# Kernel tuning notes

Measured on AMD Instinct MI355X. Metric: run time of the kernel, lower is better.

The kernel has to match this reference:

```python
import jax, jax.numpy as jnp
import numpy as np

DIM = 128
KS = 7
HEADS = 4
HEAD_DIM = DIM // HEADS


def setup_inputs() -> dict:
    key = jax.random.key(0)
    ks = jax.random.split(key, 10)
    B, H, W, C = 4, 64, 64, DIM
    s = 0.02
    return {
        "x": jax.random.normal(ks[0], (B, H, W, C), jnp.float32),
        "qkv_w": jax.random.normal(ks[1], (C, 3 * C), jnp.float32) * s,
        "qkv_b": jnp.zeros((3 * C,), jnp.float32),
        "proj_w": jax.random.normal(ks[2], (C, C), jnp.float32) * s,
        "proj_b": jnp.zeros((C,), jnp.float32),
        "rpb": jax.random.normal(ks[3], (HEADS, 2 * KS - 1, 2 * KS - 1), jnp.float32) * s,
        "g1_w": jax.random.normal(ks[4], (C, C // 2), jnp.float32) * s,
        "g1_b": jnp.zeros((C // 2,), jnp.float32),
        "g2_w": jax.random.normal(ks[5], (C // 2, 1), jnp.float32) * s,
        "g2_b": jnp.zeros((1,), jnp.float32),
    }


def _neighborhood_attention(x, qkv_w, qkv_b, proj_w, proj_b, rpb):
    B, H, W, C = x.shape
    k = KS
    # qkv projection -> [B,H,W,3,heads,head_dim]
    qkv = (x @ qkv_w + qkv_b).reshape(B, H, W, 3, HEADS, HEAD_DIM)
    q = qkv[..., 0, :, :] * (HEAD_DIM ** -0.5)  # [B,H,W,h,d]
    kk = qkv[..., 1, :, :]
    v = qkv[..., 2, :, :]

    # Clamped sliding-window start indices (NATTEN semantics)
    sh = jnp.clip(jnp.arange(H) - k // 2, 0, H - k)  # [H]
    sw = jnp.clip(jnp.arange(W) - k // 2, 0, W - k)  # [W]
    idx_h = sh[:, None] + jnp.arange(k)[None, :]  # [H,k]
    idx_w = sw[:, None] + jnp.arange(k)[None, :]  # [W,k]

    # Gather neighborhood windows: [B,H,W,k,k,h,d]
    kwin = kk[:, idx_h[:, None, :, None], idx_w[None, :, None, :]]
    vwin = v[:, idx_h[:, None, :, None], idx_w[None, :, None, :]]

    # Relative position bias indices: (neighbor - query) + (k-1)
    bih = idx_h - jnp.arange(H)[:, None] + (k - 1)  # [H,k]
    biw = idx_w - jnp.arange(W)[:, None] + (k - 1)  # [W,k]
    # bias: [h,H,W,k,k] -> [H,W,h,k,k]
    bias = rpb[:, bih[:, None, :, None], biw[None, :, None, :]]
    bias = jnp.transpose(bias, (1, 2, 0, 3, 4))

    # scores: [B,H,W,h,k,k]
    scores = jnp.einsum('bxyhd,bxyklhd->bxyhkl', q, kwin) + bias[None]
    attn = jax.nn.softmax(scores.reshape(B, H, W, HEADS, k * k), axis=-1)
    attn = attn.reshape(B, H, W, HEADS, k, k)
    out = jnp.einsum('bxyhkl,bxyklhd->bxyhd', attn, vwin).reshape(B, H, W, C)
    return out @ proj_w + proj_b


def reference(x, qkv_w, qkv_b, proj_w, proj_b, rpb, g1_w, g1_b, g2_w, g2_b):
    attn_out = _neighborhood_attention(x, qkv_w, qkv_b, proj_w, proj_b, rpb)
    gate = jax.nn.sigmoid(jax.nn.relu(x @ g1_w + g1_b) @ g2_w + g2_b)  # [B,H,W,1]
    return attn_out * gate + x
```

## Files before the change

### kernel.cpp

```cpp
#include <hip/hip_runtime.h>
#include <hip/hip_bf16.h>
#include <math.h>

#define PIXELS 16384
#define C      128
#define KS     7
#define HEADS  4
#define HD     32
#define QSCALE 0.17677669529663687f

typedef __bf16 bf16x8 __attribute__((ext_vector_type(8)));
typedef __bf16 bf16x2 __attribute__((ext_vector_type(2)));
typedef float  f32x4  __attribute__((ext_vector_type(4)));
typedef float  f32x2  __attribute__((ext_vector_type(2)));

__device__ inline unsigned short f2bf(float f) {
    unsigned int u = __builtin_bit_cast(unsigned int, f);
    u += 0x7FFFu + ((u >> 16) & 1u);
    return (unsigned short)(u >> 16);
}
__device__ inline float bflo(unsigned int u) {
    return __builtin_bit_cast(float, u << 16);
}
__device__ inline float bfhi(unsigned int u) {
    return __builtin_bit_cast(float, u & 0xFFFF0000u);
}

__global__ __launch_bounds__(256) void prep_kernel(
    const float* __restrict__ qkv_w, const float* __restrict__ g1_w,
    const float* __restrict__ qkv_b, const float* __restrict__ g1_b,
    const float* __restrict__ proj_w,
    unsigned short* __restrict__ wT, unsigned short* __restrict__ pT,
    float* __restrict__ bias_ext)
{
    const int blk = blockIdx.x, tid = threadIdx.x;
    if (blk < 56) {
        int n = blk * 8 + (tid >> 5);
        int kq = tid & 31;
        float f0, f1, f2, f3;
        if (n < 384) {
            f0 = qkv_w[(kq*4+0)*384 + n]; f1 = qkv_w[(kq*4+1)*384 + n];
            f2 = qkv_w[(kq*4+2)*384 + n]; f3 = qkv_w[(kq*4+3)*384 + n];
        } else {
            int nn = n - 384;
            f0 = g1_w[(kq*4+0)*64 + nn]; f1 = g1_w[(kq*4+1)*64 + nn];
            f2 = g1_w[(kq*4+2)*64 + nn]; f3 = g1_w[(kq*4+3)*64 + nn];
        }
        ushort4 o; o.x = f2bf(f0); o.y = f2bf(f1); o.z = f2bf(f2); o.w = f2bf(f3);
        *(ushort4*)(wT + n*128 + kq*4) = o;
    } else if (blk < 72) {
        int n = (blk - 56) * 8 + (tid >> 5);
        int kq = tid & 31;
        ushort4 o;
        o.x = f2bf(proj_w[(kq*4+0)*128 + n]);
        o.y = f2bf(proj_w[(kq*4+1)*128 + n]);
        o.z = f2bf(proj_w[(kq*4+2)*128 + n]);
        o.w = f2bf(proj_w[(kq*4+3)*128 + n]);
        *(ushort4*)(pT + n*128 + kq*4) = o;
    } else {
        for (int idx = tid; idx < 448; idx += 256)
            bias_ext[idx] = (idx < 384) ? qkv_b[idx] : g1_b[idx - 384];
    }
}

__global__ __launch_bounds__(256) void gemm_qkvh_fused(
    const float* __restrict__ x, const unsigned short* __restrict__ wT,
    const float* __restrict__ bias_ext, const float* __restrict__ g2_w,
    const float* __restrict__ g2_b, unsigned short* __restrict__ qkvb,
    float* __restrict__ gate)
{
    __shared__ __align__(16) unsigned short As[64*128];
    __shared__ __align__(16) unsigned short Bs[64*128];
    __shared__ __align__(16) unsigned short Cs[64*64];
    const int grp = blockIdx.x;
    const int ntBeg = grp ? 4 : 0, ntEnd = grp ? 7 : 4;
    const int m0 = blockIdx.y * 64;
    const int tid = threadIdx.x;

#pragma unroll
    for (int it = 0; it < 4; it++) {
        int idx = tid + it*256, row = idx >> 4, c = idx & 15;
        const float* src = x + (size_t)(m0+row)*128 + c*8;
        float4 a = *(const float4*)src;
        float4 b2 = *(const float4*)(src + 4);
        uint4 v;
        v.x = (unsigned int)f2bf(a.x)  | ((unsigned int)f2bf(a.y)  << 16);
        v.y = (unsigned int)f2bf(a.z)  | ((unsigned int)f2bf(a.w)  << 16);
        v.z = (unsigned int)f2bf(b2.x) | ((unsigned int)f2bf(b2.y) << 16);
        v.w = (unsigned int)f2bf(b2.z) | ((unsigned int)f2bf(b2.w) << 16);
        *(uint4*)(As + row*128 + ((c ^ (row&7)) << 3)) = v;
    }

    const int wave = tid >> 6, lane = tid & 63;
    const int l15 = lane & 15, quad = lane >> 4;
    const int wm = (wave & 1) * 32, wn = (wave >> 1) * 32;

    for (int nt = ntBeg; nt < ntEnd; nt++) {
        const int n0 = nt * 64;
#pragma unroll
        for (int it = 0; it < 4; it++) {
            int idx = tid + it*256, row = idx >> 4, c = idx & 15;
            uint4 v = *(const uint4*)(wT + (size_t)(n0+row)*128 + c*8);
            *(uint4*)(Bs + row*128 + ((c ^ (row&7)) << 3)) = v;
        }
        __syncthreads();

        f32x4 acc[2][2] = {};
#pragma unroll
        for (int ks = 0; ks < 4; ks++) {
            bf16x8 af[2], bq[2];
#pragma unroll
            for (int mt = 0; mt < 2; mt++) {
                int m = wm + mt*16 + l15;
                af[mt] = *(const bf16x8*)(As + m*128 + (((ks*4+quad) ^ (m&7)) << 3));
            }
#pragma unroll
            for (int ntl = 0; ntl < 2; ntl++) {
                int n = wn + ntl*16 + l15;
                bq[ntl] = *(const bf16x8*)(Bs + n*128 + (((ks*4+quad) ^ (n&7)) << 3));
            }
#pragma unroll
            for (int mt = 0; mt < 2; mt++)
#pragma unroll
                for (int ntl = 0; ntl < 2; ntl++)
                    acc[mt][ntl] = __builtin_amdgcn_mfma_f32_16x16x32_bf16(
                        af[mt], bq[ntl], acc[mt][ntl], 0, 0, 0);
        }

        if (nt < 6) {
#pragma unroll
            for (int ntl = 0; ntl < 2; ntl++) {
                int nl = wn + ntl*16 + l15;
                int ng = n0 + nl;
                float qs = (ng < 128) ? QSCALE : 1.0f;
                float bv = bias_ext[ng];
#pragma unroll
                for (int mt = 0; mt < 2; mt++)
#pragma unroll
                    for (int r = 0; r < 4; r++) {
                        int ml = wm + mt*16 + quad*4 + r;
                        Cs[ml*64 + nl] = f2bf((acc[mt][ntl][r] + bv) * qs);
                    }
            }
            __syncthreads();
            int row = tid >> 2, part = tid & 3;
            uint4 a = *(const uint4*)(Cs + row*64 + part*16);
            uint4 b = *(const uint4*)(Cs + row*64 + part*16 + 8);
            unsigned short* dst = qkvb + (size_t)(m0+row)*384 + n0 + part*16;
            *(uint4*)dst = a;
            *(uint4*)(dst + 8) = b;
        } else {
            float* gpart = (float*)Cs;
            float rs[2][4];
#pragma unroll
            for (int mt = 0; mt < 2; mt++)
#pragma unroll
                for (int r = 0; r < 4; r++) rs[mt][r] = 0.0f;
#pragma unroll
            for (int ntl = 0; ntl < 2; ntl++) {
                int nl = wn + ntl*16 + l15;
                float bv = bias_ext[384 + nl];
                float gw = g2_w[nl];
#pragma unroll
                for (int mt = 0; mt < 2; mt++)
#pragma unroll
                    for (int r = 0; r < 4; r++) {
                        float h = acc[mt][ntl][r] + bv;
                        rs[mt][r] += fmaxf(h, 0.0f) * gw;
                    }
            }
#pragma unroll
            for (int off = 1; off <= 8; off <<= 1)
#pragma unroll
                for (int mt = 0; mt < 2; mt++)
#pragma unroll
                    for (int r = 0; r < 4; r++)
                        rs[mt][r] += __shfl_xor(rs[mt][r], off);
            if (l15 == 0) {
#pragma unroll
                for (int mt = 0; mt < 2; mt++)
#pragma unroll
                    for (int r = 0; r < 4; r++)
                        gpart[(wave >> 1)*64 + wm + mt*16 + quad*4 + r] = rs[mt][r];
            }
            __syncthreads();
            if (tid < 64) {
                float g = gpart[tid] + gpart[64 + tid] + g2_b[0];
                gate[m0 + tid] = 1.0f / (1.0f + __expf(-g));
            }
        }
    }
}

__global__ __launch_bounds__(128) void attn_kernel(
    const unsigned short* __restrict__ qkvb, const float* __restrict__ rpb,
    unsigned short* __restrict__ attnb)
{
    __shared__ __align__(16) unsigned short kvs[140 * 136];
    __shared__ float rpb_lds[2 * 169];

    const int blk = blockIdx.x;
    const int pr = blk & 1;
    const int tile = (blk >> 1) & 127;
    const int b = blk >> 8;
    const int ti0 = (tile >> 3) * 4, tj0 = (tile & 7) * 8;
    int wr0 = ti0 - 3; wr0 = wr0 < 0 ? 0 : (wr0 > 54 ? 54 : wr0);
    int wc0 = tj0 - 3; wc0 = wc0 < 0 ? 0 : (wc0 > 50 ? 50 : wc0);

    const int tid = threadIdx.x;
    const int hh = tid >> 6, lane = tid & 63;
    const int h = pr * 2 + hh;
    const int half = lane >> 5;
    const int p5 = lane & 31;
    const int pi = p5 >> 3, pj = p5 & 7;
    const int i = ti0 + pi, j = tj0 + pj;
    int sh = i - 3; sh = sh < 0 ? 0 : (sh > 57 ? 57 : sh);
    int sw = j - 3; sw = sw < 0 ? 0 : (sw > 57 ? 57 : sw);
    const int dr = sh - wr0, dc = sw - wc0;
    const size_t gp = (size_t)(((b << 6) + i) << 6) + j;

    unsigned int qu[8];
    const unsigned short* qptr = qkvb + gp * 384 + h * 32 + half * 16;
    *(uint4*)(qu + 0) = *(const uint4*)(qptr + 0);
    *(uint4*)(qu + 4) = *(const uint4*)(qptr + 8);

    float rpb_v[3];
#pragma unroll
    for (int t = 0; t < 3; t++) {
        int idx = tid + t * 128;
        rpb_v[t] = (idx < 338) ? rpb[pr * 338 + idx] : 0.0f;
    }

    for (int idx = tid; idx < 140 * 16; idx += 128) {
        int pos = idx >> 4, t = idx & 15;
        int wr = pos / 14, wc = pos - wr * 14;
        size_t gpos = (size_t)(((b << 6) + (wr0 + wr)) << 6) + (wc0 + wc);
        int src = 128 + ((t >> 3) << 7) + pr * 64 + ((t & 7) << 3);
        uint4 v = *(const uint4*)(qkvb + gpos * 384 + src);
        *(uint4*)(kvs + pos * 136 + ((t >> 3) << 6) + ((t & 7) << 3)) = v;
    }
#pragma unroll
    for (int t = 0; t < 3; t++) {
        int idx = tid + t * 128;
        if (idx < 338) rpb_lds[idx] = rpb_v[t];
    }
    __syncthreads();

    f32x2 acc2[8];
#pragma unroll
    for (int p = 0; p < 8; p++) acc2[p] = (f32x2){0.f, 0.f};
    float ssum = 0.0f;

    const float* rl = rpb_lds + hh * 169;
    const int rbase = (sh - i + 6) * 13 + (sw - j + 6);
    const int hwbase = (dr * 14 + dc) * 136 + hh * 32 + half * 16;

    for (int kr = 0; kr < 7; kr++) {
        const unsigned short* rowp = kvs + hwbase + kr * (14 * 136);
        const int ri = rbase + kr * 13;

        unsigned int ku[8], vu[8];
        *(uint4*)(ku + 0) = *(const uint4*)(rowp + 0);
        *(uint4*)(ku + 4) = *(const uint4*)(rowp + 8);
        *(uint4*)(vu + 0) = *(const uint4*)(rowp + 64);
        *(uint4*)(vu + 4) = *(const uint4*)(rowp + 72);

#pragma unroll
        for (int kc = 0; kc < 7; kc++) {
            unsigned int ku2[8], vu2[8];
            if (kc < 6) {
                const unsigned short* kpn = rowp + (kc + 1) * 136;
                *(uint4*)(ku2 + 0) = *(const uint4*)(kpn + 0);
                *(uint4*)(ku2 + 4) = *(const uint4*)(kpn + 8);
                *(uint4*)(vu2 + 0) = *(const uint4*)(kpn + 64);
                *(uint4*)(vu2 + 4) = *(const uint4*)(kpn + 72);
            }

            float s0 = 0.0f, s1 = 0.0f;
#if __has_builtin(__builtin_amdgcn_fdot2_f32_bf16)
#pragma unroll
            for (int p = 0; p < 4; p++) {
                s0 = __builtin_amdgcn_fdot2_f32_bf16(
                        __builtin_bit_cast(bf16x2, qu[p]),
                        __builtin_bit_cast(bf16x2, ku[p]), s0, false);
                s1 = __builtin_amdgcn_fdot2_f32_bf16(
                        __builtin_bit_cast(bf16x2, qu[p+4]),
                        __builtin_bit_cast(bf16x2, ku[p+4]), s1, false);
            }
#else
#pragma unroll
            for (int p = 0; p < 4; p++) {
                s0 += bflo(qu[p])   * bflo(ku[p])   + bfhi(qu[p])   * bfhi(ku[p]);
                s1 += bflo(qu[p+4]) * bflo(ku[p+4]) + bfhi(qu[p+4]) * bfhi(ku[p+4]);
            }
#endif
            float s = s0 + s1;
            s += __shfl_xor(s, 32);
            float e = __expf(s + rl[ri + kc]);
            ssum += e;

            f32x2 e2 = {e, e};
#pragma unroll
            for (int p = 0; p < 8; p++) {
                f32x2 v2 = {bflo(vu[p]), bfhi(vu[p])};
                acc2[p] += e2 * v2;
            }

            if (kc < 6) {
#pragma unroll
                for (int p = 0; p < 8; p++) { ku[p] = ku2[p]; vu[p] = vu2[p]; }
            }
        }
    }

    const float inv = 1.0f / ssum;
    unsigned int o[8];
#pragma unroll
    for (int p = 0; p < 8; p++) {
        unsigned int lo = f2bf(acc2[p].x * inv);
        unsigned int hi = f2bf(acc2[p].y * inv);
        o[p] = lo | (hi << 16);
    }
    unsigned short* op = attnb + gp * 128 + h * 32 + half * 16;
    *(uint4*)(op + 0) = *(const uint4*)(o + 0);
    *(uint4*)(op + 8) = *(const uint4*)(o + 4);
}

__global__ __launch_bounds__(256) void gemm_proj_mfma(
    const unsigned short* __restrict__ ab, const unsigned short* __restrict__ pT,
    const float* __restrict__ proj_b, const float* __restrict__ gate,
    const float* __restrict__ x, float* __restrict__ out)
{
    __shared__ __align__(16) unsigned short As[64*128];
    __shared__ __align__(16) unsigned short Bs[64*128];
    const int n0 = blockIdx.x * 64;
    const int m0 = blockIdx.y * 64;
    const int tid = threadIdx.x;

#pragma unroll
    for (int it = 0; it < 4; it++) {
        int idx = tid + it*256, row = idx >> 4, c = idx & 15;
        uint4 v = *(const uint4*)(ab + (size_t)(m0+row)*128 + c*8);
        *(uint4*)(As + row*128 + ((c ^ (row&7)) << 3)) = v;
    }
#pragma unroll
    for (int it = 0; it < 4; it++) {
        int idx = tid + it*256, row = idx >> 4, c = idx & 15;
        uint4 v = *(const uint4*)(pT + (size_t)(n0+row)*128 + c*8);
        *(uint4*)(Bs + row*128 + ((c ^ (row&7)) << 3)) = v;
    }
    __syncthreads();

    const int wave = tid >> 6, lane = tid & 63;
    const int l15 = lane & 15, quad = lane >> 4;
    const int wm = (wave & 1) * 32, wn = (wave >> 1) * 32;

    f32x4 acc[2][2] = {};
#pragma unroll
    for (int ks = 0; ks < 4; ks++) {
        bf16x8 af[2], bq[2];
#pragma unroll
        for (int mt = 0; mt < 2; mt++) {
            int m = wm + mt*16 + l15;
            af[mt] = *(const bf16x8*)(As + m*128 + (((ks*4+quad) ^ (m&7)) << 3));
        }
#pragma unroll
        for (int ntl = 0; ntl < 2; ntl++) {
            int n = wn + ntl*16 + l15;
            bq[ntl] = *(const bf16x8*)(Bs + n*128 + (((ks*4+quad) ^ (n&7)) << 3));
        }
#pragma unroll
        for (int mt = 0; mt < 2; mt++)
#pragma unroll
            for (int ntl = 0; ntl < 2; ntl++)
                acc[mt][ntl] = __builtin_amdgcn_mfma_f32_16x16x32_bf16(
                    af[mt], bq[ntl], acc[mt][ntl], 0, 0, 0);
    }
    __syncthreads();

    float* Cs = (float*)As;
#pragma unroll
    for (int ntl = 0; ntl < 2; ntl++) {
        int nl = wn + ntl*16 + l15;
        float bv = proj_b[n0 + nl];
#pragma unroll
        for (int mt = 0; mt < 2; mt++)
#pragma unroll
            for (int r = 0; r < 4; r++) {
                int ml = wm + mt*16 + quad*4 + r;
                Cs[ml*64 + nl] = acc[mt][ntl][r] + bv;
            }
    }
    __syncthreads();
    int row = tid >> 2, part = tid & 3;
    float gv = gate[m0 + row];
    const float* xr = x + (size_t)(m0+row)*128 + n0 + part*16;
    float* orow = out + (size_t)(m0+row)*128 + n0 + part*16;
#pragma unroll
    for (int q = 0; q < 4; q++) {
        float4 cv = *(const float4*)(Cs + row*64 + part*16 + q*4);
        float4 xv = *(const float4*)(xr + q*4);
        float4 o;
        o.x = cv.x * gv + xv.x; o.y = cv.y * gv + xv.y;
        o.z = cv.z * gv + xv.z; o.w = cv.w * gv + xv.w;
        *(float4*)(orow + q*4) = o;
    }
}

extern "C" void kernel_launch(void* const* d_in, const int* in_sizes, int n_in,
                              void* d_out, int out_size, void* d_ws, size_t ws_size,
                              hipStream_t stream)
{
    const float* x      = (const float*)d_in[0];
    const float* qkv_w  = (const float*)d_in[1];
    const float* qkv_b  = (const float*)d_in[2];
    const float* proj_w = (const float*)d_in[3];
    const float* proj_b = (const float*)d_in[4];
    const float* rpb    = (const float*)d_in[5];
    const float* g1_w   = (const float*)d_in[6];
    const float* g1_b   = (const float*)d_in[7];
    const float* g2_w   = (const float*)d_in[8];
    const float* g2_b   = (const float*)d_in[9];
    float* out = (float*)d_out;

    float* ws        = (float*)d_ws;
    float* gate      = ws;
    float* bias_ext  = gate + 16384;
    unsigned short* wT    = (unsigned short*)(bias_ext + 448);
    unsigned short* pT    = wT + 57344;
    unsigned short* qkvb  = pT + 16384;
    unsigned short* attnb = qkvb + 6291456;

    (void)in_sizes; (void)n_in; (void)out_size; (void)ws_size;

    prep_kernel<<<73, 256, 0, stream>>>(qkv_w, g1_w, qkv_b, g1_b, proj_w,
                                        wT, pT, bias_ext);
    gemm_qkvh_fused<<<dim3(2, 256), 256, 0, stream>>>(x, wT, bias_ext,
                                                      g2_w, g2_b, qkvb, gate);
    attn_kernel<<<1024, 128, 0, stream>>>(qkvb, rpb, attnb);
    gemm_proj_mfma<<<dim3(2, 256), 256, 0, stream>>>(attnb, pT, proj_b, gate, x, out);
}
```

Baseline: 115.4 us.

## Fuse attention with output projection and inline weight conversion into GEMMs

Drops the separate weight-prep kernel. Each GEMM block now reads fp32 weights and converts them to transposed bf16 in shared memory itself. The attention kernel is merged with the output projection: each 512-thread block handles an 8x8 pixel tile across all four heads, writes the attention output to shared memory and runs the projection MFMA plus gate/residual epilogue in place. This removes two launches and the round trip of the attention buffer through global memory, at the cost of a large dynamic shared-memory footprint, fewer blocks (256) and redundant weight conversion in every block.

```diff
diff --git a/kernel.cpp b/kernel.cpp
--- a/kernel.cpp
+++ b/kernel.cpp
@@ -1,5 +1,4 @@
 #include <hip/hip_runtime.h>
-#include <hip/hip_bf16.h>
 #include <math.h>
 
 #define PIXELS 16384
@@ -26,48 +25,12 @@
     return __builtin_bit_cast(float, u & 0xFFFF0000u);
 }
 
-__global__ __launch_bounds__(256) void prep_kernel(
-    const float* __restrict__ qkv_w, const float* __restrict__ g1_w,
-    const float* __restrict__ qkv_b, const float* __restrict__ g1_b,
-    const float* __restrict__ proj_w,
-    unsigned short* __restrict__ wT, unsigned short* __restrict__ pT,
-    float* __restrict__ bias_ext)
-{
-    const int blk = blockIdx.x, tid = threadIdx.x;
-    if (blk < 56) {
-        int n = blk * 8 + (tid >> 5);
-        int kq = tid & 31;
-        float f0, f1, f2, f3;
-        if (n < 384) {
-            f0 = qkv_w[(kq*4+0)*384 + n]; f1 = qkv_w[(kq*4+1)*384 + n];
-            f2 = qkv_w[(kq*4+2)*384 + n]; f3 = qkv_w[(kq*4+3)*384 + n];
-        } else {
-            int nn = n - 384;
-            f0 = g1_w[(kq*4+0)*64 + nn]; f1 = g1_w[(kq*4+1)*64 + nn];
-            f2 = g1_w[(kq*4+2)*64 + nn]; f3 = g1_w[(kq*4+3)*64 + nn];
-        }
-        ushort4 o; o.x = f2bf(f0); o.y = f2bf(f1); o.z = f2bf(f2); o.w = f2bf(f3);
-        *(ushort4*)(wT + n*128 + kq*4) = o;
-    } else if (blk < 72) {
-        int n = (blk - 56) * 8 + (tid >> 5);
-        int kq = tid & 31;
-        ushort4 o;
-        o.x = f2bf(proj_w[(kq*4+0)*128 + n]);
-        o.y = f2bf(proj_w[(kq*4+1)*128 + n]);
-        o.z = f2bf(proj_w[(kq*4+2)*128 + n]);
-        o.w = f2bf(proj_w[(kq*4+3)*128 + n]);
-        *(ushort4*)(pT + n*128 + kq*4) = o;
-    } else {
-        for (int idx = tid; idx < 448; idx += 256)
-            bias_ext[idx] = (idx < 384) ? qkv_b[idx] : g1_b[idx - 384];
-    }
-}
-
-__global__ __launch_bounds__(256) void gemm_qkvh_fused(
-    const float* __restrict__ x, const unsigned short* __restrict__ wT,
-    const float* __restrict__ bias_ext, const float* __restrict__ g2_w,
-    const float* __restrict__ g2_b, unsigned short* __restrict__ qkvb,
-    float* __restrict__ gate)
+__global__ __launch_bounds__(256) void gemm_qkvh(
+    const float* __restrict__ x,
+    const float* __restrict__ qkv_w, const float* __restrict__ qkv_b,
+    const float* __restrict__ g1_w, const float* __restrict__ g1_b,
+    const float* __restrict__ g2_w, const float* __restrict__ g2_b,
+    unsigned short* __restrict__ qkvb, float* __restrict__ gate)
 {
     __shared__ __align__(16) unsigned short As[64*128];
     __shared__ __align__(16) unsigned short Bs[64*128];
@@ -95,13 +58,32 @@
     const int l15 = lane & 15, quad = lane >> 4;
     const int wm = (wave & 1) * 32, wn = (wave >> 1) * 32;
 
+    const int kp = tid >> 2;
+    const int nc = (tid & 3) * 16;
+    const int bchunk = kp >> 2;
+    const int boff = 2 * (kp & 3);
+
     for (int nt = ntBeg; nt < ntEnd; nt++) {
         const int n0 = nt * 64;
-#pragma unroll
-        for (int it = 0; it < 4; it++) {
-            int idx = tid + it*256, row = idx >> 4, c = idx & 15;
-            uint4 v = *(const uint4*)(wT + (size_t)(n0+row)*128 + c*8);
-            *(uint4*)(Bs + row*128 + ((c ^ (row&7)) << 3)) = v;
+        {
+            const float* r0 = (nt < 6) ? (qkv_w + (size_t)(2*kp)*384 + n0 + nc)
+                                       : (g1_w  + (size_t)(2*kp)*64  + nc);
+            const float* r1 = r0 + ((nt < 6) ? 384 : 64);
+            float e0[16], e1[16];
+#pragma unroll
+            for (int q = 0; q < 4; q++) {
+                float4 a = ((const float4*)r0)[q];
+                float4 b2 = ((const float4*)r1)[q];
+                e0[q*4+0]=a.x; e0[q*4+1]=a.y; e0[q*4+2]=a.z; e0[q*4+3]=a.w;
+                e1[q*4+0]=b2.x; e1[q*4+1]=b2.y; e1[q*4+2]=b2.z; e1[q*4+3]=b2.w;
+            }
+#pragma unroll
+            for (int i = 0; i < 16; i++) {
+                int n = nc + i;
+                unsigned int w = (unsigned int)f2bf(e0[i])
+                               | ((unsigned int)f2bf(e1[i]) << 16);
+                *(unsigned int*)(Bs + n*128 + ((bchunk ^ (n&7)) << 3) + boff) = w;
+            }
         }
         __syncthreads();
 
@@ -133,7 +115,7 @@
                 int nl = wn + ntl*16 + l15;
                 int ng = n0 + nl;
                 float qs = (ng < 128) ? QSCALE : 1.0f;
-                float bv = bias_ext[ng];
+                float bv = qkv_b[ng];
 #pragma unroll
                 for (int mt = 0; mt < 2; mt++)
 #pragma unroll
@@ -159,7 +141,7 @@
 #pragma unroll
             for (int ntl = 0; ntl < 2; ntl++) {
                 int nl = wn + ntl*16 + l15;
-                float bv = bias_ext[384 + nl];
+                float bv = g1_b[nl];
                 float gw = g2_w[nl];
 #pragma unroll
                 for (int mt = 0; mt < 2; mt++)
@@ -192,27 +174,37 @@
     }
 }
 
-__global__ __launch_bounds__(128) void attn_kernel(
+#define ATTN_PROJ_LDS (196*264*2 + 676*4 + 64*128*2 + 128*128*2)
+
+__global__ __launch_bounds__(512) void attn_proj(
     const unsigned short* __restrict__ qkvb, const float* __restrict__ rpb,
-    unsigned short* __restrict__ attnb)
+    const float* __restrict__ proj_w, const float* __restrict__ proj_b,
+    const float* __restrict__ gate, const float* __restrict__ x,
+    float* __restrict__ out)
 {
-    __shared__ __align__(16) unsigned short kvs[140 * 136];
-    __shared__ float rpb_lds[2 * 169];
-
-    const int blk = blockIdx.x;
-    const int pr = blk & 1;
-    const int tile = (blk >> 1) & 127;
-    const int b = blk >> 8;
-    const int ti0 = (tile >> 3) * 4, tj0 = (tile & 7) * 8;
-    int wr0 = ti0 - 3; wr0 = wr0 < 0 ? 0 : (wr0 > 54 ? 54 : wr0);
+    extern __shared__ __align__(16) unsigned char dynsmem[];
+    unsigned short* kvs = (unsigned short*)dynsmem;
+    float* rpb_lds = (float*)(dynsmem + 196*264*2);
+    unsigned short* As = (unsigned short*)(dynsmem + 196*264*2 + 676*4);
+    unsigned short* Bs = (unsigned short*)(dynsmem + 196*264*2 + 676*4 + 64*128*2);
+    float* Cs = (float*)dynsmem;
+
+    const int bid = blockIdx.x;
+    const int ti = bid & 7;
+    const int rest = bid >> 3;
+    const int b = rest >> 3;
+    const int tj = rest & 7;
+    const int ti0 = ti * 8, tj0 = tj * 8;
+    int wr0 = ti0 - 3; wr0 = wr0 < 0 ? 0 : (wr0 > 50 ? 50 : wr0);
     int wc0 = tj0 - 3; wc0 = wc0 < 0 ? 0 : (wc0 > 50 ? 50 : wc0);
 
     const int tid = threadIdx.x;
-    const int hh = tid >> 6, lane = tid & 63;
-    const int h = pr * 2 + hh;
+    const int wave = tid >> 6, lane = tid & 63;
+    const int h = wave & 3;
+    const int pg = wave >> 2;
     const int half = lane >> 5;
     const int p5 = lane & 31;
-    const int pi = p5 >> 3, pj = p5 & 7;
+    const int pi = pg * 4 + (p5 >> 3), pj = p5 & 7;
     const int i = ti0 + pi, j = tj0 + pj;
     int sh = i - 3; sh = sh < 0 ? 0 : (sh > 57 ? 57 : sh);
     int sw = j - 3; sw = sw < 0 ? 0 : (sw > 57 ? 57 : sw);
@@ -224,25 +216,48 @@
     *(uint4*)(qu + 0) = *(const uint4*)(qptr + 0);
     *(uint4*)(qu + 4) = *(const uint4*)(qptr + 8);
 
-    float rpb_v[3];
-#pragma unroll
-    for (int t = 0; t < 3; t++) {
-        int idx = tid + t * 128;
-        rpb_v[t] = (idx < 338) ? rpb[pr * 338 + idx] : 0.0f;
-    }
-
-    for (int idx = tid; idx < 140 * 16; idx += 128) {
-        int pos = idx >> 4, t = idx & 15;
+    float rpb_v[2];
+#pragma unroll
+    for (int t = 0; t < 2; t++) {
+        int idx = tid + t * 512;
+        rpb_v[t] = (idx < 676) ? rpb[idx] : 0.0f;
+    }
+
+    for (int idx = tid; idx < 196 * 32; idx += 512) {
+        int pos = idx >> 5, t = idx & 31;
         int wr = pos / 14, wc = pos - wr * 14;
         size_t gpos = (size_t)(((b << 6) + (wr0 + wr)) << 6) + (wc0 + wc);
-        int src = 128 + ((t >> 3) << 7) + pr * 64 + ((t & 7) << 3);
-        uint4 v = *(const uint4*)(qkvb + gpos * 384 + src);
-        *(uint4*)(kvs + pos * 136 + ((t >> 3) << 6) + ((t & 7) << 3)) = v;
-    }
-#pragma unroll
-    for (int t = 0; t < 3; t++) {
-        int idx = tid + t * 128;
-        if (idx < 338) rpb_lds[idx] = rpb_v[t];
+        uint4 v = *(const uint4*)(qkvb + gpos * 384 + 128 + t * 8);
+        *(uint4*)(kvs + pos * 264 + t * 8) = v;
+    }
+
+    {
+        const int kp = tid >> 3;
+        const int nc = (tid & 7) * 16;
+        const int bchunk = kp >> 2;
+        const int boff = 2 * (kp & 3);
+        const float* r0 = proj_w + (size_t)(2*kp)*128 + nc;
+        const float* r1 = r0 + 128;
+        float e0[16], e1[16];
+#pragma unroll
+        for (int q = 0; q < 4; q++) {
+            float4 a = ((const float4*)r0)[q];
+            float4 b2 = ((const float4*)r1)[q];
+            e0[q*4+0]=a.x; e0[q*4+1]=a.y; e0[q*4+2]=a.z; e0[q*4+3]=a.w;
+            e1[q*4+0]=b2.x; e1[q*4+1]=b2.y; e1[q*4+2]=b2.z; e1[q*4+3]=b2.w;
+        }
+#pragma unroll
+        for (int q = 0; q < 16; q++) {
+            int n = nc + q;
+            unsigned int w = (unsigned int)f2bf(e0[q])
+                           | ((unsigned int)f2bf(e1[q]) << 16);
+            *(unsigned int*)(Bs + n*128 + ((bchunk ^ (n&7)) << 3) + boff) = w;
+        }
+    }
+#pragma unroll
+    for (int t = 0; t < 2; t++) {
+        int idx = tid + t * 512;
+        if (idx < 676) rpb_lds[idx] = rpb_v[t];
     }
     __syncthreads();
 
@@ -251,29 +266,29 @@
     for (int p = 0; p < 8; p++) acc2[p] = (f32x2){0.f, 0.f};
     float ssum = 0.0f;
 
-    const float* rl = rpb_lds + hh * 169;
+    const float* rl = rpb_lds + h * 169;
     const int rbase = (sh - i + 6) * 13 + (sw - j + 6);
-    const int hwbase = (dr * 14 + dc) * 136 + hh * 32 + half * 16;
+    const int hwbase = (dr * 14 + dc) * 264 + h * 32 + half * 16;
 
     for (int kr = 0; kr < 7; kr++) {
-        const unsigned short* rowp = kvs + hwbase + kr * (14 * 136);
+        const unsigned short* rowp = kvs + hwbase + kr * (14 * 264);
         const int ri = rbase + kr * 13;
 
         unsigned int ku[8], vu[8];
         *(uint4*)(ku + 0) = *(const uint4*)(rowp + 0);
         *(uint4*)(ku + 4) = *(const uint4*)(rowp + 8);
-        *(uint4*)(vu + 0) = *(const uint4*)(rowp + 64);
-        *(uint4*)(vu + 4) = *(const uint4*)(rowp + 72);
+        *(uint4*)(vu + 0) = *(const uint4*)(rowp + 128);
+        *(uint4*)(vu + 4) = *(const uint4*)(rowp + 136);
 
 #pragma unroll
         for (int kc = 0; kc < 7; kc++) {
             unsigned int ku2[8], vu2[8];
             if (kc < 6) {
-                const unsigned short* kpn = rowp + (kc + 1) * 136;
+                const unsigned short* kpn = rowp + (kc + 1) * 264;
                 *(uint4*)(ku2 + 0) = *(const uint4*)(kpn + 0);
                 *(uint4*)(ku2 + 4) = *(const uint4*)(kpn + 8);
-                *(uint4*)(vu2 + 0) = *(const uint4*)(kpn + 64);
-                *(uint4*)(vu2 + 4) = *(const uint4*)(kpn + 72);
+                *(uint4*)(vu2 + 0) = *(const uint4*)(kpn + 128);
+                *(uint4*)(vu2 + 4) = *(const uint4*)(kpn + 136);
             }
 
             float s0 = 0.0f, s1 = 0.0f;
@@ -313,97 +328,79 @@
         }
     }
 
-    const float inv = 1.0f / ssum;
-    unsigned int o[8];
-#pragma unroll
-    for (int p = 0; p < 8; p++) {
-        unsigned int lo = f2bf(acc2[p].x * inv);
-        unsigned int hi = f2bf(acc2[p].y * inv);
-        o[p] = lo | (hi << 16);
-    }
-    unsigned short* op = attnb + gp * 128 + h * 32 + half * 16;
-    *(uint4*)(op + 0) = *(const uint4*)(o + 0);
-    *(uint4*)(op + 8) = *(const uint4*)(o + 4);
-}
-
-__global__ __launch_bounds__(256) void gemm_proj_mfma(
-    const unsigned short* __restrict__ ab, const unsigned short* __restrict__ pT,
-    const float* __restrict__ proj_b, const float* __restrict__ gate,
-    const float* __restrict__ x, float* __restrict__ out)
-{
-    __shared__ __align__(16) unsigned short As[64*128];
-    __shared__ __align__(16) unsigned short Bs[64*128];
-    const int n0 = blockIdx.x * 64;
-    const int m0 = blockIdx.y * 64;
-    const int tid = threadIdx.x;
-
-#pragma unroll
-    for (int it = 0; it < 4; it++) {
-        int idx = tid + it*256, row = idx >> 4, c = idx & 15;
-        uint4 v = *(const uint4*)(ab + (size_t)(m0+row)*128 + c*8);
-        *(uint4*)(As + row*128 + ((c ^ (row&7)) << 3)) = v;
-    }
-#pragma unroll
-    for (int it = 0; it < 4; it++) {
-        int idx = tid + it*256, row = idx >> 4, c = idx & 15;
-        uint4 v = *(const uint4*)(pT + (size_t)(n0+row)*128 + c*8);
-        *(uint4*)(Bs + row*128 + ((c ^ (row&7)) << 3)) = v;
+    {
+        const float inv = 1.0f / ssum;
+        unsigned int o[8];
+#pragma unroll
+        for (int p = 0; p < 8; p++) {
+            unsigned int lo = f2bf(acc2[p].x * inv);
+            unsigned int hi = f2bf(acc2[p].y * inv);
+            o[p] = lo | (hi << 16);
+        }
+        const int pix = pi * 8 + pj;
+        const int c0 = h * 4 + half * 2;
+        *(uint4*)(As + pix*128 + (((c0  ) ^ (pix&7)) << 3)) = *(const uint4*)(o + 0);
+        *(uint4*)(As + pix*128 + (((c0+1) ^ (pix&7)) << 3)) = *(const uint4*)(o + 4);
     }
     __syncthreads();
 
-    const int wave = tid >> 6, lane = tid & 63;
-    const int l15 = lane & 15, quad = lane >> 4;
-    const int wm = (wave & 1) * 32, wn = (wave >> 1) * 32;
-
-    f32x4 acc[2][2] = {};
-#pragma unroll
-    for (int ks = 0; ks < 4; ks++) {
-        bf16x8 af[2], bq[2];
-#pragma unroll
-        for (int mt = 0; mt < 2; mt++) {
-            int m = wm + mt*16 + l15;
-            af[mt] = *(const bf16x8*)(As + m*128 + (((ks*4+quad) ^ (m&7)) << 3));
-        }
+    {
+        const int l15 = lane & 15, quad = lane >> 4;
+        const int wm = (wave & 1) * 32, wn = (wave >> 1) * 32;
+
+        f32x4 acc[2][2] = {};
+#pragma unroll
+        for (int ks = 0; ks < 4; ks++) {
+            bf16x8 af[2], bq[2];
+#pragma unroll
+            for (int mt = 0; mt < 2; mt++) {
+                int m = wm + mt*16 + l15;
+                af[mt] = *(const bf16x8*)(As + m*128 + (((ks*4+quad) ^ (m&7)) << 3));
+            }
+#pragma unroll
+            for (int ntl = 0; ntl < 2; ntl++) {
+                int n = wn + ntl*16 + l15;
+                bq[ntl] = *(const bf16x8*)(Bs + n*128 + (((ks*4+quad) ^ (n&7)) << 3));
+            }
+#pragma unroll
+            for (int mt = 0; mt < 2; mt++)
+#pragma unroll
+                for (int ntl = 0; ntl < 2; ntl++)
+                    acc[mt][ntl] = __builtin_amdgcn_mfma_f32_16x16x32_bf16(
+                        af[mt], bq[ntl], acc[mt][ntl], 0, 0, 0);
+        }
+
 #pragma unroll
         for (int ntl = 0; ntl < 2; ntl++) {
-            int n = wn + ntl*16 + l15;
-            bq[ntl] = *(const bf16x8*)(Bs + n*128 + (((ks*4+quad) ^ (n&7)) << 3));
-        }
-#pragma unroll
-        for (int mt = 0; mt < 2; mt++)
-#pragma unroll
-            for (int ntl = 0; ntl < 2; ntl++)
-                acc[mt][ntl] = __builtin_amdgcn_mfma_f32_16x16x32_bf16(
-                    af[mt], bq[ntl], acc[mt][ntl], 0, 0, 0);
+            int nl = wn + ntl*16 + l15;
+            float bv = proj_b[nl];
+#pragma unroll
+            for (int mt = 0; mt < 2; mt++)
+#pragma unroll
+                for (int r = 0; r < 4; r++) {
+                    int ml = wm + mt*16 + quad*4 + r;
+                    Cs[ml*128 + nl] = acc[mt][ntl][r] + bv;
+                }
+        }
     }
     __syncthreads();
 
-    float* Cs = (float*)As;
-#pragma unroll
-    for (int ntl = 0; ntl < 2; ntl++) {
-        int nl = wn + ntl*16 + l15;
-        float bv = proj_b[n0 + nl];
-#pragma unroll
-        for (int mt = 0; mt < 2; mt++)
-#pragma unroll
-            for (int r = 0; r < 4; r++) {
-                int ml = wm + mt*16 + quad*4 + r;
-                Cs[ml*64 + nl] = acc[mt][ntl][r] + bv;
-            }
-    }
-    __syncthreads();
-    int row = tid >> 2, part = tid & 3;
-    float gv = gate[m0 + row];
-    const float* xr = x + (size_t)(m0+row)*128 + n0 + part*16;
-    float* orow = out + (size_t)(m0+row)*128 + n0 + part*16;
-#pragma unroll
-    for (int q = 0; q < 4; q++) {
-        float4 cv = *(const float4*)(Cs + row*64 + part*16 + q*4);
-        float4 xv = *(const float4*)(xr + q*4);
-        float4 o;
-        o.x = cv.x * gv + xv.x; o.y = cv.y * gv + xv.y;
-        o.z = cv.z * gv + xv.z; o.w = cv.w * gv + xv.w;
-        *(float4*)(orow + q*4) = o;
+    {
+        int pix = tid >> 3, part = tid & 7;
+        int gi = ti0 + (pix >> 3), gj = tj0 + (pix & 7);
+        size_t gr = (size_t)(((b << 6) + gi) << 6) + gj;
+        float gv = gate[gr];
+        const float* xr = x + gr*128 + part*16;
+        float* orow = out + gr*128 + part*16;
+#pragma unroll
+        for (int q = 0; q < 4; q++) {
+            float4 cv = *(const float4*)(Cs + pix*128 + part*16 + q*4);
+            float4 xv = *(const float4*)(xr + q*4);
+            float4 o;
+            o.x = cv.x * gv + xv.x; o.y = cv.y * gv + xv.y;
+            o.z = cv.z * gv + xv.z; o.w = cv.w * gv + xv.w;
+            *(float4*)(orow + q*4) = o;
+        }
     }
 }
 
@@ -425,18 +422,20 @@
 
     float* ws        = (float*)d_ws;
     float* gate      = ws;
-    float* bias_ext  = gate + 16384;
-    unsigned short* wT    = (unsigned short*)(bias_ext + 448);
-    unsigned short* pT    = wT + 57344;
-    unsigned short* qkvb  = pT + 16384;
-    unsigned short* attnb = qkvb + 6291456;
+    unsigned short* qkvb = (unsigned short*)(gate + 16384);
 
     (void)in_sizes; (void)n_in; (void)out_size; (void)ws_size;
 
-    prep_kernel<<<73, 256, 0, stream>>>(qkv_w, g1_w, qkv_b, g1_b, proj_w,
-                                        wT, pT, bias_ext);
-    gemm_qkvh_fused<<<dim3(2, 256), 256, 0, stream>>>(x, wT, bias_ext,
-                                                      g2_w, g2_b, qkvb, gate);
-    attn_kernel<<<1024, 128, 0, stream>>>(qkvb, rpb, attnb);
-    gemm_proj_mfma<<<dim3(2, 256), 256, 0, stream>>>(attnb, pT, proj_b, gate, x, out);
-}
+    static int lds_ok = -1;
+    if (lds_ok < 0) {
+        hipError_t ae = hipFuncSetAttribute(
+            (const void*)attn_proj,
+            hipFuncAttributeMaxDynamicSharedMemorySize, ATTN_PROJ_LDS);
+        lds_ok = (ae == hipSuccess) ? 1 : 0;
+    }
+
+    gemm_qkvh<<<dim3(2, 256), 256, 0, stream>>>(x, qkv_w, qkv_b, g1_w, g1_b,
+                                                g2_w, g2_b, qkvb, gate);
+    attn_proj<<<256, 512, ATTN_PROJ_LDS, stream>>>(qkvb, rpb, proj_w, proj_b,
+                                                   gate, x, out);
+}
```

Measured after the change: 114.3 us. About the same (-1.0%).
